# Kernel tuning notes

Hardware: AMD Instinct MI355X
Metric: run time of the kernel (lower is better)

Reference implementation:

```python
import jax, jax.numpy as jnp
import numpy as np

B, S, R = 32, 1024, 1024
HID, OUT = 512, 1024

def setup_inputs() -> dict:
    key = jax.random.key(0)
    k1, k2, k3, k4, k5, k6 = jax.random.split(key, 6)
    return {
        "representation": jax.random.normal(k1, (B, 1, R), dtype=jnp.float32),
        "size_matrix": jax.random.uniform(k2, (B, S, 1), dtype=jnp.float32),
        "W1": jax.random.normal(k3, (HID, R), dtype=jnp.float32) * 0.02,
        "b1": jax.random.normal(k4, (HID,), dtype=jnp.float32) * 0.02,
        "W2": jax.random.normal(k5, (OUT, HID), dtype=jnp.float32) * 0.02,
        "b2": jax.random.normal(k6, (OUT,), dtype=jnp.float32) * 0.02,
    }

def reference(representation, size_matrix, W1, b1, W2, b2):
    # bmm(ones_like(size_matrix)[B,S,1], representation[B,1,R]) == broadcast to [B,S,R]
    ones = jnp.ones_like(size_matrix)                       # [B,S,1]
    sized = jnp.einsum('bso,bor->bsr', ones, representation)  # [B,S,R]
    # per-position 2-layer MLP, fused into two batched GEMMs over all B*S positions
    h = jax.nn.relu(jnp.einsum('bsr,hr->bsh', sized, W1) + b1)  # [B,S,HID]
    out = jnp.einsum('bsh,oh->bso', h, W2) + b2                 # [B,S,OUT]
    return out
```

## Files before the change

kernel.cpp:

```cpp
#include <hip/hip_runtime.h>
#include <hip/hip_bf16.h>

#define BB  32
#define SS  1024
#define RR  1024
#define HID 512
#define OUTD 1024

__global__ __launch_bounds__(256) void layer1_kernel(
    const float* __restrict__ rep, const float* __restrict__ W1,
    const float* __restrict__ b1, float* __restrict__ h) {
  const int gwave = (blockIdx.x * 256 + threadIdx.x) >> 6;
  const int lane  = threadIdx.x & 63;
  const int b = gwave >> 9;
  const int j = gwave & (HID - 1);

  const float4* w = reinterpret_cast<const float4*>(W1 + (size_t)j * RR);
  const float4* r = reinterpret_cast<const float4*>(rep + (size_t)b * RR);
  float acc = 0.f;
#pragma unroll
  for (int t = 0; t < 4; ++t) {
    const float4 wv = w[lane + 64 * t];
    const float4 rv = r[lane + 64 * t];
    acc += wv.x * rv.x + wv.y * rv.y + wv.z * rv.z + wv.w * rv.w;
  }
  acc += __shfl_xor(acc, 1);
  acc += __shfl_xor(acc, 2);
  acc += __shfl_xor(acc, 4);
  acc += __shfl_xor(acc, 8);
  acc += __shfl_xor(acc, 16);
  acc += __shfl_xor(acc, 32);
  if (lane == 0) h[gwave] = fmaxf(acc + b1[j], 0.f);
}

__global__ __launch_bounds__(256) void layer2_kernel(
    const float* __restrict__ h, const float* __restrict__ W2,
    const float* __restrict__ b2, float* __restrict__ out) {
  const int gwave = (blockIdx.x * 256 + threadIdx.x) >> 6;
  const int lane  = threadIdx.x & 63;
  const int b = gwave >> 10;
  const int k = gwave & (OUTD - 1);

  const float4* w  = reinterpret_cast<const float4*>(W2 + (size_t)k * HID);
  const float4* hv = reinterpret_cast<const float4*>(h + (size_t)b * HID);
  float acc = 0.f;
#pragma unroll
  for (int t = 0; t < 2; ++t) {
    const float4 wv = w[lane + 64 * t];
    const float4 xv = hv[lane + 64 * t];
    acc += wv.x * xv.x + wv.y * xv.y + wv.z * xv.z + wv.w * xv.w;
  }
  acc += __shfl_xor(acc, 1);
  acc += __shfl_xor(acc, 2);
  acc += __shfl_xor(acc, 4);
  acc += __shfl_xor(acc, 8);
  acc += __shfl_xor(acc, 16);
  acc += __shfl_xor(acc, 32);
  if (lane == 0) out[(size_t)b * SS * OUTD + k] = acc + b2[k];
}

__global__ __launch_bounds__(256) void bcast_kernel(float* __restrict__ out) {
  const int b     = blockIdx.x >> 6;
  const int chunk = blockIdx.x & 63;
  float4* __restrict__ base = reinterpret_cast<float4*>(out + (size_t)b * SS * OUTD);
  const float4 v = base[threadIdx.x];
  const int s0 = chunk * 16;
#pragma unroll
  for (int i = 0; i < 16; ++i) {
    const int s = s0 + i;
    if (s != 0) base[(size_t)s * (OUTD / 4) + threadIdx.x] = v;
  }
}

extern "C" void kernel_launch(void* const* d_in, const int* in_sizes, int n_in,
                              void* d_out, int out_size, void* d_ws, size_t ws_size,
                              hipStream_t stream) {
  const float* rep = (const float*)d_in[0];
  const float* W1 = (const float*)d_in[2];
  const float* b1 = (const float*)d_in[3];
  const float* W2 = (const float*)d_in[4];
  const float* b2 = (const float*)d_in[5];
  float* out = (float*)d_out;
  float* h   = (float*)d_ws;

  layer1_kernel<<<BB * HID / 4, 256, 0, stream>>>(rep, W1, b1, h);
  layer2_kernel<<<BB * OUTD / 4, 256, 0, stream>>>(h, W2, b2, out);
  bcast_kernel<<<BB * 64, 256, 0, stream>>>(out);
}
```

Before: 39.51 us.

## Fuse layer-2 matvec with broadcast write into one kernel

```diff
diff --git a/kernel.cpp b/kernel.cpp
--- a/kernel.cpp
+++ b/kernel.cpp
@@ -33,42 +33,50 @@
   if (lane == 0) h[gwave] = fmaxf(acc + b1[j], 0.f);
 }
 
-__global__ __launch_bounds__(256) void layer2_kernel(
+__global__ __launch_bounds__(256) void layer2_bcast_kernel(
     const float* __restrict__ h, const float* __restrict__ W2,
     const float* __restrict__ b2, float* __restrict__ out) {
-  const int gwave = (blockIdx.x * 256 + threadIdx.x) >> 6;
-  const int lane  = threadIdx.x & 63;
-  const int b = gwave >> 10;
-  const int k = gwave & (OUTD - 1);
+  __shared__ float s_h[HID];
+  __shared__ float s_o[256];
+  const int tid  = threadIdx.x;
+  const int b    = blockIdx.x >> 4;
+  const int c    = (blockIdx.x >> 2) & 3;
+  const int q    = blockIdx.x & 3;
+  const int wave = tid >> 6;
+  const int lane = tid & 63;
 
-  const float4* w  = reinterpret_cast<const float4*>(W2 + (size_t)k * HID);
-  const float4* hv = reinterpret_cast<const float4*>(h + (size_t)b * HID);
-  float acc = 0.f;
+  reinterpret_cast<float2*>(s_h)[tid] =
+      reinterpret_cast<const float2*>(h + (size_t)b * HID)[tid];
+  __syncthreads();
+
+  const int c0 = c << 8;
+  const float4* s_h4 = reinterpret_cast<const float4*>(s_h);
+#pragma unroll 4
+  for (int it = 0; it < 64; ++it) {
+    const int k = c0 + (it << 2) + wave;
+    const float4* w = reinterpret_cast<const float4*>(W2 + (size_t)k * HID);
+    const float4 w0 = w[lane], w1 = w[lane + 64];
+    const float4 h0 = s_h4[lane], h1 = s_h4[lane + 64];
+    float acc = w0.x * h0.x + w0.y * h0.y + w0.z * h0.z + w0.w * h0.w
+              + w1.x * h1.x + w1.y * h1.y + w1.z * h1.z + w1.w * h1.w;
+    acc += __shfl_xor(acc, 1);
+    acc += __shfl_xor(acc, 2);
+    acc += __shfl_xor(acc, 4);
+    acc += __shfl_xor(acc, 8);
+    acc += __shfl_xor(acc, 16);
+    acc += __shfl_xor(acc, 32);
+    if (lane == 0) s_o[(it << 2) + wave] = acc + b2[k];
+  }
+  __syncthreads();
+
+  const float4 v = reinterpret_cast<const float4*>(s_o)[lane];
+  float4* __restrict__ out4 = reinterpret_cast<float4*>(out);
+  const size_t base = ((size_t)b * SS) * (OUTD / 4) + (c << 6) + lane;
+  const int s0 = q << 8;
 #pragma unroll
-  for (int t = 0; t < 2; ++t) {
-    const float4 wv = w[lane + 64 * t];
-    const float4 xv = hv[lane + 64 * t];
-    acc += wv.x * xv.x + wv.y * xv.y + wv.z * xv.z + wv.w * xv.w;
-  }
-  acc += __shfl_xor(acc, 1);
-  acc += __shfl_xor(acc, 2);
-  acc += __shfl_xor(acc, 4);
-  acc += __shfl_xor(acc, 8);
-  acc += __shfl_xor(acc, 16);
-  acc += __shfl_xor(acc, 32);
-  if (lane == 0) out[(size_t)b * SS * OUTD + k] = acc + b2[k];
-}
-
-__global__ __launch_bounds__(256) void bcast_kernel(float* __restrict__ out) {
-  const int b     = blockIdx.x >> 6;
-  const int chunk = blockIdx.x & 63;
-  float4* __restrict__ base = reinterpret_cast<float4*>(out + (size_t)b * SS * OUTD);
-  const float4 v = base[threadIdx.x];
-  const int s0 = chunk * 16;
-#pragma unroll
-  for (int i = 0; i < 16; ++i) {
-    const int s = s0 + i;
-    if (s != 0) base[(size_t)s * (OUTD / 4) + threadIdx.x] = v;
+  for (int it = 0; it < 64; ++it) {
+    const int s = s0 + (it << 2) + wave;
+    out4[base + (size_t)s * (OUTD / 4)] = v;
   }
 }
 
@@ -84,6 +92,5 @@
   float* h   = (float*)d_ws;
 
   layer1_kernel<<<BB * HID / 4, 256, 0, stream>>>(rep, W1, b1, h);
-  layer2_kernel<<<BB * OUTD / 4, 256, 0, stream>>>(h, W2, b2, out);
-  bcast_kernel<<<BB * 64, 256, 0, stream>>>(out);
+  layer2_bcast_kernel<<<BB * 4 * 4, 256, 0, stream>>>(h, W2, b2, out);
 }
```

New measurement: 63.46 us. 1.61x slower.
